# Performance work log

Measured on AMD Instinct MI355X. Metric: run time of the kernel, lower is better.

Reference implementation:

```python
import jax, jax.numpy as jnp
import numpy as np

V, D, H = 50000, 256, 4
HD = H * D            # concat head dim (TransformerConv concat=True)
HH, O = 256, 256      # invariant_hidden_dim, invariant_out_dim
B, N, E, L, A = 16, 1000, 4000, 64, 128
PAD = 0
SCALE = 1.0 / float(np.sqrt(D))


def emb_lookup(table, idx):
    # nn.Embedding with padding_idx: forward is a plain gather; grad at pad row is zeroed.
    rows = table[idx]
    return jnp.where((idx == PAD)[..., None], jax.lax.stop_gradient(rows), rows)


def transformer_conv(x, edge_index, ea, Wq, bq, Wk, bk, Wv, bv, We, Wskip, bskip):
    # PyG TransformerConv, heads=H, concat=True, root_weight=True, beta=False, dropout=0 (eval)
    n = x.shape[0]
    src, dst = edge_index[0], edge_index[1]
    q = (x @ Wq + bq).reshape(n, H, D)
    e = (ea @ We).reshape(-1, H, D)          # lin_edge (bias=False)
    k = (x @ Wk + bk).reshape(n, H, D)[src] + e
    v = (x @ Wv + bv).reshape(n, H, D)[src] + e
    alpha = (q[dst] * k).sum(-1) * SCALE      # [E,H]
    amax = jax.ops.segment_max(alpha, dst, num_segments=n)
    ex = jnp.exp(alpha - amax[dst])
    denom = jax.ops.segment_sum(ex, dst, num_segments=n)
    w = ex / denom[dst]                       # per-target-node softmax over incoming edges
    agg = jax.ops.segment_sum(v * w[..., None], dst, num_segments=n)
    return agg.reshape(n, HD) + x @ Wskip + bskip  # lin_skip on root


def mixed_embed(tok, node, graph_repr, emb):
    fixed = emb_lookup(emb, tok)
    flex = jnp.take_along_axis(graph_repr, node[..., None], axis=1)
    flex = jnp.where((node == PAD)[..., None], jax.lax.stop_gradient(flex), flex)
    return fixed + flex


def gru_last(xs, W_ih, W_hh, b_ih, b_hh):
    # torch nn.GRU, batch_first, 1 layer; only last hidden state is used
    gx = jnp.einsum('blh,gh->blg', xs, W_ih) + b_ih  # [B,L,3O]

    def step(h, g):
        gh = h @ W_hh.T + b_hh
        xr, xz, xn = jnp.split(g, 3, axis=-1)
        hr, hz, hn = jnp.split(gh, 3, axis=-1)
        r = jax.nn.sigmoid(xr + hr)
        z = jax.nn.sigmoid(xz + hz)
        c = jnp.tanh(xn + r * hn)
        return (1.0 - z) * c + z * h, None

    h0 = jnp.zeros((xs.shape[0], W_hh.shape[1]), xs.dtype)
    h_last, _ = jax.lax.scan(step, h0, jnp.swapaxes(gx, 0, 1))
    return h_last


def setup_inputs() -> dict:
    key = jax.random.key(0)
    ks = jax.random.split(key, 40)
    f = lambda i, shape, s=0.05: jax.random.normal(ks[i], shape, jnp.float32) * s
    ri = lambda i, shape, hi: jax.random.randint(ks[i], shape, 0, hi)
    return {
        'node_tokens': ri(0, (B, N), V),
        'edge_tokens': ri(1, (B, E), V),
        'edge_index': ri(2, (B, 2, E), N),
        'inv_token': ri(3, (B, L), V),
        'inv_node': ri(4, (B, L), N),
        'aa_token': ri(5, (B, A), V),
        'aa_node': ri(6, (B, A), N),
        'action_mask': jnp.ones((B, A), jnp.float32),
        'emb': f(7, (V, D), 0.02),
        'Wq': f(8, (D, HD)), 'bq': f(9, (HD,)),
        'Wk': f(10, (D, HD)), 'bk': f(11, (HD,)),
        'Wv': f(12, (D, HD)), 'bv': f(13, (HD,)),
        'We': f(14, (D, HD)),
        'Wskip': f(15, (D, HD)), 'bskip': f(16, (HD,)),
        'W1': f(17, (HD, D)), 'b1': f(18, (D,)),
        'Wp': f(19, (D, HH)), 'bp': f(20, (HH,)),
        'W_ih': f(21, (3 * O, HH)), 'W_hh': f(22, (3 * O, O)),
        'b_ih': f(23, (3 * O,)), 'b_hh': f(24, (3 * O,)),
        'Wab': f(25, (D, 1)), 'bab': f(26, (1,)),
        'Wap': f(27, (D, O)), 'bap': f(28, (O,)),
    }


def reference(node_tokens, edge_tokens, edge_index, inv_token, inv_node, aa_token, aa_node,
              action_mask, emb, Wq, bq, Wk, bk, Wv, bv, We, Wskip, bskip, W1, b1,
              Wp, bp, W_ih, W_hh, b_ih, b_hh, Wab, bab, Wap, bap):
    x = emb_lookup(emb, node_tokens)    # [B,N,D]
    ea = emb_lookup(emb, edge_tokens)   # [B,E,D]
    conv = jax.vmap(lambda xx, ei, ee: transformer_conv(
        xx, ei, ee, Wq, bq, Wk, bk, Wv, bv, We, Wskip, bskip))
    h = jax.nn.relu(conv(x, edge_index, ea))            # [B,N,HD]
    graph_repr = jax.nn.relu(h @ W1 + b1)               # [B,N,D]
    inv_h = jax.nn.relu(mixed_embed(inv_token, inv_node, graph_repr, emb) @ Wp + bp)
    inv = gru_last(inv_h, W_ih, W_hh, b_ih, b_hh)       # [B,O]
    aa_emb = mixed_embed(aa_token, aa_node, graph_repr, emb)  # [B,A,D]
    scores = jnp.einsum('bao,bo->ba', aa_emb @ Wap + bap, inv) + (aa_emb @ Wab + bab)[..., 0]
    inf_mask = jnp.maximum(jnp.log(action_mask), jnp.float32(np.finfo(np.float32).min))
    return scores + inf_mask
```

## Files before the change

kernel.cpp:

```cpp
#include <hip/hip_runtime.h>
#include <hip/hip_bf16.h>
#include <float.h>
#include <math.h>

typedef __hip_bfloat16 bf16;

#define B_ 16
#define N_ 1000
#define E_ 4000
#define L_ 64
#define A_ 128
#define D_ 256
#define H_ 4
#define HD_ 1024
#define SCALE_ 0.0625f

typedef __attribute__((ext_vector_type(8))) short short8;
typedef __attribute__((ext_vector_type(4))) float f32x4;

union U4S8 { uint4 u; short8 s; };

__device__ __forceinline__ unsigned short f2bf(float f) {
    bf16 h = __float2bfloat16(f);
    return *reinterpret_cast<unsigned short*>(&h);
}
__device__ __forceinline__ unsigned pack2(float a, float b) {
    return (unsigned)f2bf(a) | ((unsigned)f2bf(b) << 16);
}
__device__ __forceinline__ unsigned rne2(float a, float b) {
    unsigned ua = __float_as_uint(a), ub = __float_as_uint(b);
    ua += 0x7fff + ((ua >> 16) & 1);
    ub += 0x7fff + ((ub >> 16) & 1);
    return (ua >> 16) | (ub & 0xffff0000u);
}
__device__ __forceinline__ float bflo(unsigned u) { return __uint_as_float(u << 16); }
__device__ __forceinline__ float bfhi(unsigned u) { return __uint_as_float(u & 0xffff0000u); }

#define LOG2E 1.4426950408889634f
__device__ __forceinline__ float fsigm(float x) {
    return __builtin_amdgcn_rcpf(1.f + __builtin_amdgcn_exp2f(-LOG2E * x));
}
__device__ __forceinline__ float ftanh(float x) {
    return 1.f - 2.f * __builtin_amdgcn_rcpf(1.f + __builtin_amdgcn_exp2f(2.f * LOG2E * x));
}

__global__ void convemb_kernel(const float* __restrict__ src, bf16* __restrict__ dst, long n4)
{
    long i = (long)blockIdx.x * 256 + threadIdx.x;
    if (i >= n4) return;
    float4 v = *(const float4*)(src + i * 4);
    *(uint2*)(dst + i * 4) = make_uint2(pack2(v.x, v.y), pack2(v.z, v.w));
}

__global__ void pack_all_kernel(const float* __restrict__ Wq, const float* __restrict__ Wk,
                                const float* __restrict__ Wv, const float* __restrict__ Wskip,
                                const float* __restrict__ We, const float* __restrict__ W1,
                                const float* __restrict__ Wp, const float* __restrict__ W_ih,
                                const float* __restrict__ Wap, const float* __restrict__ W_hh,
                                const float* __restrict__ bq, const float* __restrict__ bk,
                                const float* __restrict__ bv, const float* __restrict__ bskip,
                                unsigned* __restrict__ qkvsP, unsigned* __restrict__ WeP,
                                unsigned* __restrict__ W1P, unsigned* __restrict__ WpP,
                                unsigned* __restrict__ WihP, unsigned* __restrict__ WapP,
                                short8* __restrict__ WhhP, float* __restrict__ bias4096)
{
    int i = blockIdx.x * 256 + threadIdx.x;
    if (i < 524288) {
        int k2 = i >> 12, n = i & 4095;
        const float* s = (n < 1024) ? Wq : (n < 2048) ? Wk : (n < 3072) ? Wv : Wskip;
        int col = n & 1023;
        qkvsP[i] = pack2(s[(long)(2 * k2) * 1024 + col], s[(long)(2 * k2 + 1) * 1024 + col]);
        return;
    }
    i -= 524288;
    if (i < 131072) {
        int k2 = i >> 10, n = i & 1023;
        WeP[i] = pack2(We[(long)(2 * k2) * 1024 + n], We[(long)(2 * k2 + 1) * 1024 + n]);
        return;
    }
    i -= 131072;
    if (i < 131072) {
        int k2 = i >> 8, n = i & 255;
        W1P[i] = pack2(W1[(long)(2 * k2) * 256 + n], W1[(long)(2 * k2 + 1) * 256 + n]);
        return;
    }
    i -= 131072;
    if (i < 32768) {
        int k2 = i >> 8, n = i & 255;
        WpP[i] = pack2(Wp[(long)(2 * k2) * 256 + n], Wp[(long)(2 * k2 + 1) * 256 + n]);
        return;
    }
    i -= 32768;
    if (i < 98304) {
        int k2 = i / 768, n = i % 768;
        WihP[i] = pack2(W_ih[(long)n * 256 + 2 * k2], W_ih[(long)n * 256 + 2 * k2 + 1]);
        return;
    }
    i -= 98304;
    if (i < 32768) {
        int k2 = i >> 8, n = i & 255;
        WapP[i] = pack2(Wap[(long)(2 * k2) * 256 + n], Wap[(long)(2 * k2 + 1) * 256 + n]);
        return;
    }
    i -= 32768;
    if (i < 24576) {
        int lane = i & 63, tk = (i >> 6) & 7, tile = i >> 9;
        int n = tile * 16 + (lane & 15);
        const float* wp = W_hh + (long)n * 256 + tk * 32 + (lane >> 4) * 8;
        float4 w0 = *(const float4*)wp;
        float4 w1 = *(const float4*)(wp + 4);
        U4S8 u;
        u.u = make_uint4(pack2(w0.x, w0.y), pack2(w0.z, w0.w),
                         pack2(w1.x, w1.y), pack2(w1.z, w1.w));
        WhhP[i] = u.s;
        return;
    }
    i -= 24576;
    if (i < 4096) {
        int q = i >> 10, c = i & 1023;
        bias4096[i] = ((q == 0) ? bq : (q == 1) ? bk : (q == 2) ? bv : bskip)[c];
    }
}
#define PACK_ALL_TOT (524288 + 131072 + 131072 + 32768 + 98304 + 32768 + 24576 + 4096)

#define TM 128
#define TN 128
#define TK 32
#define ASTR 40
#define BSTR 132

template <typename CT>
__global__ __launch_bounds__(256)
void pgemm_kernel(const bf16* __restrict__ A, const int* __restrict__ arows,
                  const unsigned* __restrict__ Bp, const float* __restrict__ bias,
                  CT* __restrict__ C, int M, int K, int Nc, int relu_out)
{
    __shared__ short    As[TM * ASTR];
    __shared__ unsigned Bs[(TK / 2) * BSTR];

    const int tid  = threadIdx.x;
    const int lane = tid & 63;
    const int wave = tid >> 6;
    const int wm = wave >> 1, wn = wave & 1;
    const int quad = lane >> 4, c16 = lane & 15;
    const long row0 = (long)blockIdx.y * TM;
    const int  col0 = blockIdx.x * TN;

    const int sm  = tid >> 1;
    const int sh  = (tid & 1) * 16;
    const int sn2 = tid & 63;
    const int skk = (tid >> 6) * 4;

    long gr_row = row0 + sm;
    if (gr_row > M - 1) gr_row = M - 1;
    long ar = arows ? (long)arows[gr_row] : gr_row;
    const short* Arow = (const short*)A + ar * K + sh;

    f32x4 acc[4][4];
    #pragma unroll
    for (int i = 0; i < 4; ++i)
        #pragma unroll
        for (int j = 0; j < 4; ++j)
            acc[i][j] = (f32x4){0.f, 0.f, 0.f, 0.f};

    for (int k0 = 0; k0 < K; k0 += TK) {
        {
            const short* p = Arow + k0;
            uint4 a = *(const uint4*)(p);
            uint4 b = *(const uint4*)(p + 8);
            *(uint4*)&As[sm * ASTR + sh]     = a;
            *(uint4*)&As[sm * ASTR + sh + 8] = b;
        }
        #pragma unroll
        for (int i = 0; i < 4; ++i) {
            int kk2 = skk + i;
            *(uint2*)&Bs[kk2 * BSTR + sn2 * 2] =
                *(const uint2*)&Bp[(long)(k0 / 2 + kk2) * Nc + col0 + sn2 * 2];
        }
        __syncthreads();

        short8 af[4];
        U4S8   bfr[4];
        #pragma unroll
        for (int mi = 0; mi < 4; ++mi) {
            int m = wm * 64 + mi * 16 + c16;
            af[mi] = *(const short8*)&As[m * ASTR + quad * 8];
        }
        #pragma unroll
        for (int ni = 0; ni < 4; ++ni) {
            int n = wn * 64 + ni * 16 + c16;
            uint4 u;
            u.x = Bs[(quad * 4 + 0) * BSTR + n];
            u.y = Bs[(quad * 4 + 1) * BSTR + n];
            u.z = Bs[(quad * 4 + 2) * BSTR + n];
            u.w = Bs[(quad * 4 + 3) * BSTR + n];
            bfr[ni].u = u;
        }
        #pragma unroll
        for (int mi = 0; mi < 4; ++mi)
            #pragma unroll
            for (int ni = 0; ni < 4; ++ni)
                acc[mi][ni] = __builtin_amdgcn_mfma_f32_16x16x32_bf16(
                    af[mi], bfr[ni].s, acc[mi][ni], 0, 0, 0);
        __syncthreads();
    }

    #pragma unroll
    for (int ni = 0; ni < 4; ++ni) {
        int col = col0 + wn * 64 + ni * 16 + c16;
        float bv = bias ? bias[col] : 0.f;
        #pragma unroll
        for (int mi = 0; mi < 4; ++mi) {
            long row = row0 + wm * 64 + mi * 16 + quad * 4;
            #pragma unroll
            for (int r = 0; r < 4; ++r) {
                if (row + r >= M) continue;
                float v = acc[mi][ni][r] + bv;
                if (relu_out) v = fmaxf(v, 0.f);
                C[(row + r) * Nc + col] = (CT)v;
            }
        }
    }
}

__global__ void zero_int_kernel(int* __restrict__ p, int n)
{
    int i = blockIdx.x * 256 + threadIdx.x;
    if (i < n) p[i] = 0;
}

__global__ void count_kernel(const int* __restrict__ edge_index, int b0,
                             int* __restrict__ cnt, int cE)
{
    int i = blockIdx.x * 256 + threadIdx.x;
    if (i >= cE) return;
    int bl = i / E_, ei = i % E_;
    int dst = edge_index[(long)(b0 + bl) * 2 * E_ + E_ + ei];
    atomicAdd(&cnt[bl * N_ + dst], 1);
}

__global__ __launch_bounds__(1024)
void scan_kernel(const int* __restrict__ cnt, int* __restrict__ row_start,
                 int* __restrict__ cursor)
{
    int bl = blockIdx.x;
    int tid = threadIdx.x;
    __shared__ int s[1024];
    int v = (tid < N_) ? cnt[bl * N_ + tid] : 0;
    s[tid] = v;
    __syncthreads();
    for (int off = 1; off < 1024; off <<= 1) {
        int t = (tid >= off) ? s[tid - off] : 0;
        __syncthreads();
        s[tid] += t;
        __syncthreads();
    }
    if (tid < N_) {
        int excl = s[tid] - v;
        row_start[bl * N_ + tid] = excl;
        cursor[bl * N_ + tid] = excl;
    }
}

__global__ void scatter_kernel(const int* __restrict__ edge_index, int b0,
                               int* __restrict__ cursor, int* __restrict__ elist, int cE)
{
    int i = blockIdx.x * 256 + threadIdx.x;
    if (i >= cE) return;
    int bl = i / E_, ei = i % E_;
    int dst = edge_index[(long)(b0 + bl) * 2 * E_ + E_ + ei];
    int pos = atomicAdd(&cursor[bl * N_ + dst], 1);
    elist[bl * E_ + pos] = ei;
}

__device__ __forceinline__ float qke2(unsigned q, unsigned k, unsigned e)
{
    return bflo(q) * (bflo(k) + bflo(e)) + bfhi(q) * (bfhi(k) + bfhi(e));
}

__global__ void alpha_ex_kernel(const bf16* __restrict__ qkvs, const bf16* __restrict__ e,
                                const int* __restrict__ edge_index,
                                int b0, float* __restrict__ ex, int cE)
{
    int eidx = blockIdx.x * 4 + (threadIdx.x >> 6);
    int l = threadIdx.x & 63;
    int bl = eidx / E_, ei = eidx % E_;
    const int* eb = edge_index + (long)(b0 + bl) * 2 * E_;
    int src = eb[ei], dst = eb[E_ + ei];
    int head = l >> 4;
    int j0 = head * 256 + (l & 15) * 16;

    const uint4* qp = (const uint4*)(qkvs + (long)(bl * N_ + dst) * 4096 + j0);
    const uint4* kp = (const uint4*)(qkvs + (long)(bl * N_ + src) * 4096 + 1024 + j0);
    const uint4* ep = (const uint4*)(e + (long)eidx * HD_ + j0);

    uint4 qa = qp[0], qb2 = qp[1];
    uint4 ka = kp[0], kb2 = kp[1];
    uint4 ea = ep[0], eb2 = ep[1];

    float s = qke2(qa.x, ka.x, ea.x) + qke2(qa.y, ka.y, ea.y)
            + qke2(qa.z, ka.z, ea.z) + qke2(qa.w, ka.w, ea.w)
            + qke2(qb2.x, kb2.x, eb2.x) + qke2(qb2.y, kb2.y, eb2.y)
            + qke2(qb2.z, kb2.z, eb2.z) + qke2(qb2.w, kb2.w, eb2.w);

    s += __shfl_down(s, 8);
    s += __shfl_down(s, 4);
    s += __shfl_down(s, 2);
    s += __shfl_down(s, 1);

    if ((l & 15) == 0)
        ex[(long)head * cE + eidx] = expf(s * SCALE_);
}

__global__ void agg_node_kernel(const bf16* __restrict__ qkvs, const bf16* __restrict__ e,
                                const float* __restrict__ ex, const int* __restrict__ edge_index,
                                const int* __restrict__ row_start, const int* __restrict__ cnt,
                                const int* __restrict__ elist,
                                int b0, int cE, bf16* __restrict__ aggb)
{
    int base = blockIdx.x;
    int bl = base / N_;
    int tid = threadIdx.x;
    int h = tid >> 6;
    int j0 = tid * 4;

    int start = row_start[base];
    int deg = cnt[base];
    const int* el = elist + (long)bl * E_;
    const float* exh = ex + (long)h * cE;
    const int* srcp = edge_index + (long)(b0 + bl) * 2 * E_;

    float d = 0.f;
    for (int t = 0; t < deg; ++t)
        d += exh[(long)bl * E_ + el[start + t]];
    float invd = (deg > 0) ? 1.f / d : 0.f;

    float a0 = 0.f, a1 = 0.f, a2 = 0.f, a3 = 0.f;
    for (int t = 0; t < deg; ++t) {
        int ei = el[start + t];
        long eidx = (long)bl * E_ + ei;
        float w = exh[eidx] * invd;
        int src = srcp[ei];
        uint2 vv = *(const uint2*)(qkvs + (long)(bl * N_ + src) * 4096 + 2048 + j0);
        uint2 ee = *(const uint2*)(e + eidx * HD_ + j0);
        a0 += w * (bflo(vv.x) + bflo(ee.x));
        a1 += w * (bfhi(vv.x) + bfhi(ee.x));
        a2 += w * (bflo(vv.y) + bflo(ee.y));
        a3 += w * (bfhi(vv.y) + bfhi(ee.y));
    }

    uint2 sk = *(const uint2*)(qkvs + (long)base * 4096 + 3072 + j0);
    unsigned o0 = pack2(fmaxf(bflo(sk.x) + a0, 0.f), fmaxf(bfhi(sk.x) + a1, 0.f));
    unsigned o1 = pack2(fmaxf(bflo(sk.y) + a2, 0.f), fmaxf(bfhi(sk.y) + a3, 0.f));
    *(uint2*)(aggb + (long)base * HD_ + j0) = make_uint2(o0, o1);
}

__global__ void mixed2_kernel(const bf16* __restrict__ embh,
                              const int* __restrict__ inv_token, const int* __restrict__ inv_node,
                              const int* __restrict__ aa_token, const int* __restrict__ aa_node,
                              const float* __restrict__ graph_repr,
                              bf16* __restrict__ mixed_inv, bf16* __restrict__ aa_emb)
{
    int r = blockIdx.x;
    int d = threadIdx.x;
    if (r < B_ * L_) {
        int b = r / L_;
        float v = (float)embh[(long)inv_token[r] * D_ + d] +
                  graph_repr[((long)b * N_ + inv_node[r]) * D_ + d];
        mixed_inv[(long)r * D_ + d] = __float2bfloat16(v);
    } else {
        int r2 = r - B_ * L_;
        int b = r2 / A_;
        float v = (float)embh[(long)aa_token[r2] * D_ + d] +
                  graph_repr[((long)b * N_ + aa_node[r2]) * D_ + d];
        aa_emb[(long)r2 * D_ + d] = __float2bfloat16(v);
    }
}

#define GSTR 780

__global__ __launch_bounds__(1024)
void gru_kernel(const bf16* __restrict__ gxh, const short8* __restrict__ WhhP,
                const float* __restrict__ b_hh, float* __restrict__ inv_out)
{
    __shared__ float gatesLDS[16 * GSTR];
    __shared__ short hB[16 * 264];

    const int tid = threadIdx.x;
    const int lane = tid & 63;
    const int wave = tid >> 6;
    const int quad = lane >> 4, col = lane & 15;

    for (int i = tid; i < 16 * 264; i += 1024) hB[i] = 0;

    short8 wfrag[3][8];
    float bhh[3];
    #pragma unroll
    for (int i = 0; i < 3; ++i) {
        int tile = wave * 3 + i;
        bhh[i] = b_hh[tile * 16 + col];
        #pragma unroll
        for (int tk = 0; tk < 8; ++tk)
            wfrag[i][tk] = WhhP[(tile * 8 + tk) * 64 + lane];
    }

    const int em = tid >> 6;
    const int c0 = (tid & 63) * 4;
    float myh0 = 0.f, myh1 = 0.f, myh2 = 0.f, myh3 = 0.f;

    const short* gbase = (const short*)gxh + (long)em * L_ * 768 + c0;

    uint2 pxr = *(const uint2*)(gbase);
    uint2 pxz = *(const uint2*)(gbase + 256);
    uint2 pxn = *(const uint2*)(gbase + 512);

    __syncthreads();

    for (int t = 0; t < L_; ++t) {
        uint2 xr2 = pxr, xz2 = pxz, xn2 = pxn;
        int nxt = (t + 1 < L_) ? t + 1 : t;
        const short* gp = gbase + (long)nxt * 768;
        pxr = *(const uint2*)(gp);
        pxz = *(const uint2*)(gp + 256);
        pxn = *(const uint2*)(gp + 512);

        f32x4 acc0 = (f32x4){bhh[0], bhh[0], bhh[0], bhh[0]};
        f32x4 acc1 = (f32x4){bhh[1], bhh[1], bhh[1], bhh[1]};
        f32x4 acc2 = (f32x4){bhh[2], bhh[2], bhh[2], bhh[2]};
        #pragma unroll
        for (int tk = 0; tk < 8; ++tk) {
            short8 a = *(const short8*)&hB[col * 264 + tk * 32 + quad * 8];
            acc0 = __builtin_amdgcn_mfma_f32_16x16x32_bf16(a, wfrag[0][tk], acc0, 0, 0, 0);
            acc1 = __builtin_amdgcn_mfma_f32_16x16x32_bf16(a, wfrag[1][tk], acc1, 0, 0, 0);
            acc2 = __builtin_amdgcn_mfma_f32_16x16x32_bf16(a, wfrag[2][tk], acc2, 0, 0, 0);
        }
        #pragma unroll
        for (int r = 0; r < 4; ++r) {
            int m = quad * 4 + r;
            gatesLDS[m * GSTR + (wave * 3 + 0) * 16 + col] = acc0[r];
            gatesLDS[m * GSTR + (wave * 3 + 1) * 16 + col] = acc1[r];
            gatesLDS[m * GSTR + (wave * 3 + 2) * 16 + col] = acc2[r];
        }
        __syncthreads();

        const float* g = &gatesLDS[em * GSTR + c0];
        float4 grv = *(const float4*)(g);
        float4 gzv = *(const float4*)(g + 256);
        float4 gnv = *(const float4*)(g + 512);
        float gr[4] = {grv.x, grv.y, grv.z, grv.w};
        float gz[4] = {gzv.x, gzv.y, gzv.z, gzv.w};
        float gn[4] = {gnv.x, gnv.y, gnv.z, gnv.w};
        float xr[4] = {bflo(xr2.x), bfhi(xr2.x), bflo(xr2.y), bfhi(xr2.y)};
        float xz[4] = {bflo(xz2.x), bfhi(xz2.x), bflo(xz2.y), bfhi(xz2.y)};
        float xn[4] = {bflo(xn2.x), bfhi(xn2.x), bflo(xn2.y), bfhi(xn2.y)};
        float hn[4];
        float hold[4] = {myh0, myh1, myh2, myh3};
        #pragma unroll
        for (int j = 0; j < 4; ++j) {
            float r = fsigm(xr[j] + gr[j]);
            float z = fsigm(xz[j] + gz[j]);
            float cc = ftanh(xn[j] + r * gn[j]);
            hn[j] = (1.f - z) * cc + z * hold[j];
        }
        myh0 = hn[0]; myh1 = hn[1]; myh2 = hn[2]; myh3 = hn[3];
        *(uint2*)&hB[em * 264 + c0] =
            make_uint2(rne2(hn[0], hn[1]), rne2(hn[2], hn[3]));
        __syncthreads();
    }

    float* op = inv_out + (long)em * 256 + c0;
    *(float4*)op = make_float4(myh0, myh1, myh2, myh3);
}

__global__ void score_kernel(const float* __restrict__ aa_p, const bf16* __restrict__ aa_emb,
                             const float* __restrict__ inv, const float* __restrict__ Wab,
                             const float* __restrict__ bab, const float* __restrict__ mask,
                             float* __restrict__ out)
{
    int r = blockIdx.x * 4 + (threadIdx.x >> 6);
    int l = threadIdx.x & 63;
    int b = r / A_;
    float s = 0.f;
    for (int d = l; d < D_; d += 64)
        s += aa_p[(long)r * D_ + d] * inv[(long)b * D_ + d] +
             (float)aa_emb[(long)r * D_ + d] * Wab[d];
    #pragma unroll
    for (int off = 32; off; off >>= 1) s += __shfl_down(s, off);
    if (l == 0) {
        float lm = logf(mask[r]);
        const float MN = -3.4028234663852886e38f;
        if (!(lm >= MN)) lm = MN;
        out[r] = s + bab[0] + lm;
    }
}

static inline size_t align256(size_t x) { return (x + 255) & ~(size_t)255; }

template <typename CT>
static void launch_pgemm(const bf16* A, const int* arows, const unsigned* Bp,
                         const float* bias, CT* C, int M, int K, int Nc, int relu,
                         hipStream_t s)
{
    dim3 grid(Nc / TN, (M + TM - 1) / TM);
    pgemm_kernel<CT><<<grid, 256, 0, s>>>(A, arows, Bp, bias, C, M, K, Nc, relu);
}

extern "C" void kernel_launch(void* const* d_in, const int* in_sizes, int n_in,
                              void* d_out, int out_size, void* d_ws, size_t ws_size,
                              hipStream_t stream)
{
    const int* node_tokens = (const int*)d_in[0];
    const int* edge_tokens = (const int*)d_in[1];
    const int* edge_index  = (const int*)d_in[2];
    const int* inv_token   = (const int*)d_in[3];
    const int* inv_node    = (const int*)d_in[4];
    const int* aa_token    = (const int*)d_in[5];
    const int* aa_node     = (const int*)d_in[6];
    const float* action_mask = (const float*)d_in[7];
    const float* emb   = (const float*)d_in[8];
    const float* Wq    = (const float*)d_in[9];
    const float* bq    = (const float*)d_in[10];
    const float* Wk    = (const float*)d_in[11];
    const float* bk    = (const float*)d_in[12];
    const float* Wv    = (const float*)d_in[13];
    const float* bv    = (const float*)d_in[14];
    const float* We    = (const float*)d_in[15];
    const float* Wskip = (const float*)d_in[16];
    const float* bskip = (const float*)d_in[17];
    const float* W1    = (const float*)d_in[18];
    const float* b1    = (const float*)d_in[19];
    const float* Wp    = (const float*)d_in[20];
    const float* bp    = (const float*)d_in[21];
    const float* W_ih  = (const float*)d_in[22];
    const float* W_hh  = (const float*)d_in[23];
    const float* b_ih  = (const float*)d_in[24];
    const float* b_hh  = (const float*)d_in[25];
    const float* Wab   = (const float*)d_in[26];
    const float* bab   = (const float*)d_in[27];
    const float* Wap   = (const float*)d_in[28];
    const float* bap   = (const float*)d_in[29];
    (void)in_sizes; (void)n_in; (void)out_size;

    char* base = (char*)d_ws;
    size_t off = 0;
    auto alloc = [&](size_t bytes) -> char* {
        char* p = base + off;
        off = align256(off + bytes);
        return p;
    };

    const long VD = 50000L * 256;
    bf16*  embh       = (bf16*)alloc(VD * 2);
    float* graph_repr = (float*)alloc((size_t)B_ * N_ * D_ * 4);
    bf16*  mixed_inv  = (bf16*)alloc((size_t)B_ * L_ * D_ * 2);
    bf16*  inv_h      = (bf16*)alloc((size_t)B_ * L_ * D_ * 2);
    bf16*  gxh        = (bf16*)alloc((size_t)B_ * L_ * 768 * 2);
    float* inv_out    = (float*)alloc((size_t)B_ * 256 * 4);
    bf16*  aa_emb     = (bf16*)alloc((size_t)B_ * A_ * D_ * 2);
    float* aa_p       = (float*)alloc((size_t)B_ * A_ * 256 * 4);
    unsigned* qkvsP   = (unsigned*)alloc((size_t)128 * 4096 * 4);
    unsigned* WeP     = (unsigned*)alloc((size_t)128 * 1024 * 4);
    unsigned* W1P     = (unsigned*)alloc((size_t)512 * 256 * 4);
    unsigned* WpP     = (unsigned*)alloc((size_t)128 * 256 * 4);
    unsigned* WihP    = (unsigned*)alloc((size_t)128 * 768 * 4);
    unsigned* WapP    = (unsigned*)alloc((size_t)128 * 256 * 4);
    short8* WhhP      = (short8*)alloc((size_t)24576 * 16);
    float* bias4096   = (float*)alloc(4096 * 4);
    size_t persist = off;

    int c = 16;
    while (c > 1) {
        size_t cN = (size_t)c * N_, cEs = (size_t)c * E_;
        size_t chunk = align256(cN * 4096 * 2)
                     + align256(cEs * HD_ * 2)
                     + align256(cN * HD_ * 2)
                     + align256(cEs * H_ * 4)
                     + 3 * align256(cN * 4)
                     + align256(cEs * 4);
        if (persist + chunk <= ws_size) break;
        c >>= 1;
    }
    int cN = c * N_, cE = c * E_;

    bf16*  qkvs  = (bf16*)alloc((size_t)cN * 4096 * 2);
    bf16*  ebuf  = (bf16*)alloc((size_t)cE * HD_ * 2);
    bf16*  aggb  = (bf16*)alloc((size_t)cN * HD_ * 2);
    float* ex    = (float*)alloc((size_t)cE * H_ * 4);
    int*   cnt   = (int*)alloc((size_t)cN * 4);
    int*   rstart= (int*)alloc((size_t)cN * 4);
    int*   cursor= (int*)alloc((size_t)cN * 4);
    int*   elist = (int*)alloc((size_t)cE * 4);

    convemb_kernel<<<(int)((VD / 4 + 255) / 256), 256, 0, stream>>>(emb, embh, VD / 4);
    pack_all_kernel<<<(PACK_ALL_TOT + 255) / 256, 256, 0, stream>>>(
        Wq, Wk, Wv, Wskip, We, W1, Wp, W_ih, Wap, W_hh, bq, bk, bv, bskip,
        qkvsP, WeP, W1P, WpP, WihP, WapP, WhhP, bias4096);

    for (int b0 = 0; b0 < B_; b0 += c) {
        zero_int_kernel<<<(cN + 255) / 256, 256, 0, stream>>>(cnt, cN);
        count_kernel<<<(cE + 255) / 256, 256, 0, stream>>>(edge_index, b0, cnt, cE);
        scan_kernel<<<c, 1024, 0, stream>>>(cnt, rstart, cursor);
        scatter_kernel<<<(cE + 255) / 256, 256, 0, stream>>>(edge_index, b0, cursor,
                                                             elist, cE);
        launch_pgemm<bf16>(embh, node_tokens + (long)b0 * N_, qkvsP, bias4096, qkvs,
                           cN, D_, 4096, 0, stream);
        launch_pgemm<bf16>(embh, edge_tokens + (long)b0 * E_, WeP, nullptr, ebuf,
                           cE, D_, HD_, 0, stream);
        alpha_ex_kernel<<<cE / 4, 256, 0, stream>>>(qkvs, ebuf, edge_index, b0, ex, cE);
        agg_node_kernel<<<cN, 256, 0, stream>>>(qkvs, ebuf, ex, edge_index, rstart, cnt,
                                                elist, b0, cE, aggb);
        launch_pgemm<float>(aggb, nullptr, W1P, b1,
                            graph_repr + (long)b0 * N_ * D_, cN, HD_, D_, 1, stream);
    }

    mixed2_kernel<<<B_ * L_ + B_ * A_, 256, 0, stream>>>(embh, inv_token, inv_node,
                                                         aa_token, aa_node, graph_repr,
                                                         mixed_inv, aa_emb);
    launch_pgemm<bf16>(mixed_inv, nullptr, WpP, bp, inv_h, B_ * L_, D_, 256, 1, stream);
    launch_pgemm<bf16>(inv_h, nullptr, WihP, b_ih, gxh, B_ * L_, 256, 768, 0, stream);
    gru_kernel<<<1, 1024, 0, stream>>>(gxh, WhhP, b_hh, inv_out);

    launch_pgemm<float>(aa_emb, nullptr, WapP, bap, aa_p, B_ * A_, D_, 256, 0, stream);
    score_kernel<<<(B_ * A_) / 4, 256, 0, stream>>>(aa_p, aa_emb, inv_out, Wab, bab,
                                                    action_mask, (float*)d_out);
}
```

Baseline: 906.9 us.

## Restructure GRU to compute gates in-register and double-buffer hidden state

The GRU kernel is reorganised so each wave owns matching r/z/n column tiles. Gate nonlinearities are then applied directly on the MFMA accumulators, which removes the gates LDS round trip and one of the two barriers per timestep. The hidden state is double-buffered in LDS, and a new transpose kernel lays out the input gates time-major with batch innermost to match the accumulator layout. The softmax exponential also switches from expf to the native exp2. This adds an extra launch and scattered 2-byte LDS writes.

```diff
diff --git a/kernel.cpp b/kernel.cpp
--- a/kernel.cpp
+++ b/kernel.cpp
@@ -27,11 +27,10 @@
 __device__ __forceinline__ unsigned pack2(float a, float b) {
     return (unsigned)f2bf(a) | ((unsigned)f2bf(b) << 16);
 }
-__device__ __forceinline__ unsigned rne2(float a, float b) {
-    unsigned ua = __float_as_uint(a), ub = __float_as_uint(b);
+__device__ __forceinline__ unsigned short rne1(float a) {
+    unsigned ua = __float_as_uint(a);
     ua += 0x7fff + ((ua >> 16) & 1);
-    ub += 0x7fff + ((ub >> 16) & 1);
-    return (ua >> 16) | (ub & 0xffff0000u);
+    return (unsigned short)(ua >> 16);
 }
 __device__ __forceinline__ float bflo(unsigned u) { return __uint_as_float(u << 16); }
 __device__ __forceinline__ float bfhi(unsigned u) { return __uint_as_float(u & 0xffff0000u); }
@@ -123,6 +122,16 @@
 }
 #define PACK_ALL_TOT (524288 + 131072 + 131072 + 32768 + 98304 + 32768 + 24576 + 4096)
 
+__global__ void gxt_kernel(const bf16* __restrict__ gxh, bf16* __restrict__ gxT)
+{
+    int i = blockIdx.x * 256 + threadIdx.x;
+    if (i >= B_ * L_ * 768) return;
+    int b = i / (L_ * 768);
+    int rem = i - b * (L_ * 768);
+    int t = rem / 768, n = rem - (rem / 768) * 768;
+    gxT[((long)t * 768 + n) * 16 + b] = gxh[i];
+}
+
 #define TM 128
 #define TN 128
 #define TK 32
@@ -309,7 +318,7 @@
     s += __shfl_down(s, 1);
 
     if ((l & 15) == 0)
-        ex[(long)head * cE + eidx] = expf(s * SCALE_);
+        ex[(long)head * cE + eidx] = __builtin_amdgcn_exp2f(s * (SCALE_ * LOG2E));
 }
 
 __global__ void agg_node_kernel(const bf16* __restrict__ qkvs, const bf16* __restrict__ e,
@@ -377,99 +386,86 @@
     }
 }
 
-#define GSTR 780
-
 __global__ __launch_bounds__(1024)
-void gru_kernel(const bf16* __restrict__ gxh, const short8* __restrict__ WhhP,
+void gru_kernel(const bf16* __restrict__ gxT, const short8* __restrict__ WhhP,
                 const float* __restrict__ b_hh, float* __restrict__ inv_out)
 {
-    __shared__ float gatesLDS[16 * GSTR];
-    __shared__ short hB[16 * 264];
+    __shared__ short hB[2][16 * 264];
 
     const int tid = threadIdx.x;
     const int lane = tid & 63;
     const int wave = tid >> 6;
-    const int quad = lane >> 4, col = lane & 15;
-
-    for (int i = tid; i < 16 * 264; i += 1024) hB[i] = 0;
-
-    short8 wfrag[3][8];
-    float bhh[3];
+    const int quad = lane >> 4, c16 = lane & 15;
+    const int n0 = wave * 16 + c16;
+
+    for (int i = tid; i < 2 * 16 * 264; i += 1024) ((short*)hB)[i] = 0;
+
+    short8 wfr[8], wfz[8], wfn[8];
     #pragma unroll
-    for (int i = 0; i < 3; ++i) {
-        int tile = wave * 3 + i;
-        bhh[i] = b_hh[tile * 16 + col];
-        #pragma unroll
-        for (int tk = 0; tk < 8; ++tk)
-            wfrag[i][tk] = WhhP[(tile * 8 + tk) * 64 + lane];
-    }
-
-    const int em = tid >> 6;
-    const int c0 = (tid & 63) * 4;
+    for (int tk = 0; tk < 8; ++tk) {
+        wfr[tk] = WhhP[((0 * 16 + wave) * 8 + tk) * 64 + lane];
+        wfz[tk] = WhhP[((1 * 16 + wave) * 8 + tk) * 64 + lane];
+        wfn[tk] = WhhP[((2 * 16 + wave) * 8 + tk) * 64 + lane];
+    }
+    float bhr = b_hh[0 * 256 + n0];
+    float bhz = b_hh[1 * 256 + n0];
+    float bhn = b_hh[2 * 256 + n0];
+
     float myh0 = 0.f, myh1 = 0.f, myh2 = 0.f, myh3 = 0.f;
 
-    const short* gbase = (const short*)gxh + (long)em * L_ * 768 + c0;
-
-    uint2 pxr = *(const uint2*)(gbase);
-    uint2 pxz = *(const uint2*)(gbase + 256);
-    uint2 pxn = *(const uint2*)(gbase + 512);
+    const short* gbr = (const short*)gxT + (long)(0 * 256 + n0) * 16 + quad * 4;
+    const short* gbz = gbr + 256 * 16;
+    const short* gbn = gbr + 512 * 16;
+
+    uint2 pxr = *(const uint2*)gbr;
+    uint2 pxz = *(const uint2*)gbz;
+    uint2 pxn = *(const uint2*)gbn;
 
     __syncthreads();
 
+    int p = 0;
     for (int t = 0; t < L_; ++t) {
         uint2 xr2 = pxr, xz2 = pxz, xn2 = pxn;
-        int nxt = (t + 1 < L_) ? t + 1 : t;
-        const short* gp = gbase + (long)nxt * 768;
-        pxr = *(const uint2*)(gp);
-        pxz = *(const uint2*)(gp + 256);
-        pxn = *(const uint2*)(gp + 512);
-
-        f32x4 acc0 = (f32x4){bhh[0], bhh[0], bhh[0], bhh[0]};
-        f32x4 acc1 = (f32x4){bhh[1], bhh[1], bhh[1], bhh[1]};
-        f32x4 acc2 = (f32x4){bhh[2], bhh[2], bhh[2], bhh[2]};
+        long noff = (long)((t + 1 < L_) ? t + 1 : t) * 12288;
+        pxr = *(const uint2*)(gbr + noff);
+        pxz = *(const uint2*)(gbz + noff);
+        pxn = *(const uint2*)(gbn + noff);
+
+        f32x4 ar = (f32x4){bhr, bhr, bhr, bhr};
+        f32x4 az = (f32x4){bhz, bhz, bhz, bhz};
+        f32x4 an = (f32x4){bhn, bhn, bhn, bhn};
+        const short* hp = &hB[p][0];
         #pragma unroll
         for (int tk = 0; tk < 8; ++tk) {
-            short8 a = *(const short8*)&hB[col * 264 + tk * 32 + quad * 8];
-            acc0 = __builtin_amdgcn_mfma_f32_16x16x32_bf16(a, wfrag[0][tk], acc0, 0, 0, 0);
-            acc1 = __builtin_amdgcn_mfma_f32_16x16x32_bf16(a, wfrag[1][tk], acc1, 0, 0, 0);
-            acc2 = __builtin_amdgcn_mfma_f32_16x16x32_bf16(a, wfrag[2][tk], acc2, 0, 0, 0);
+            short8 a = *(const short8*)&hp[c16 * 264 + tk * 32 + quad * 8];
+            ar = __builtin_amdgcn_mfma_f32_16x16x32_bf16(a, wfr[tk], ar, 0, 0, 0);
+            az = __builtin_amdgcn_mfma_f32_16x16x32_bf16(a, wfz[tk], az, 0, 0, 0);
+            an = __builtin_amdgcn_mfma_f32_16x16x32_bf16(a, wfn[tk], an, 0, 0, 0);
         }
-        #pragma unroll
-        for (int r = 0; r < 4; ++r) {
-            int m = quad * 4 + r;
-            gatesLDS[m * GSTR + (wave * 3 + 0) * 16 + col] = acc0[r];
-            gatesLDS[m * GSTR + (wave * 3 + 1) * 16 + col] = acc1[r];
-            gatesLDS[m * GSTR + (wave * 3 + 2) * 16 + col] = acc2[r];
-        }
-        __syncthreads();
-
-        const float* g = &gatesLDS[em * GSTR + c0];
-        float4 grv = *(const float4*)(g);
-        float4 gzv = *(const float4*)(g + 256);
-        float4 gnv = *(const float4*)(g + 512);
-        float gr[4] = {grv.x, grv.y, grv.z, grv.w};
-        float gz[4] = {gzv.x, gzv.y, gzv.z, gzv.w};
-        float gn[4] = {gnv.x, gnv.y, gnv.z, gnv.w};
+
         float xr[4] = {bflo(xr2.x), bfhi(xr2.x), bflo(xr2.y), bfhi(xr2.y)};
         float xz[4] = {bflo(xz2.x), bfhi(xz2.x), bflo(xz2.y), bfhi(xz2.y)};
         float xn[4] = {bflo(xn2.x), bfhi(xn2.x), bflo(xn2.y), bfhi(xn2.y)};
+        float hold[4] = {myh0, myh1, myh2, myh3};
         float hn[4];
-        float hold[4] = {myh0, myh1, myh2, myh3};
-        #pragma unroll
-        for (int j = 0; j < 4; ++j) {
-            float r = fsigm(xr[j] + gr[j]);
-            float z = fsigm(xz[j] + gz[j]);
-            float cc = ftanh(xn[j] + r * gn[j]);
-            hn[j] = (1.f - z) * cc + z * hold[j];
+        short* hw = &hB[p ^ 1][0];
+        #pragma unroll
+        for (int r = 0; r < 4; ++r) {
+            float rr = fsigm(xr[r] + ar[r]);
+            float zz = fsigm(xz[r] + az[r]);
+            float cc = ftanh(xn[r] + rr * an[r]);
+            hn[r] = (1.f - zz) * cc + zz * hold[r];
+            hw[(quad * 4 + r) * 264 + n0] = (short)rne1(hn[r]);
         }
         myh0 = hn[0]; myh1 = hn[1]; myh2 = hn[2]; myh3 = hn[3];
-        *(uint2*)&hB[em * 264 + c0] =
-            make_uint2(rne2(hn[0], hn[1]), rne2(hn[2], hn[3]));
+        p ^= 1;
         __syncthreads();
     }
 
-    float* op = inv_out + (long)em * 256 + c0;
-    *(float4*)op = make_float4(myh0, myh1, myh2, myh3);
+    inv_out[(long)(quad * 4 + 0) * 256 + n0] = myh0;
+    inv_out[(long)(quad * 4 + 1) * 256 + n0] = myh1;
+    inv_out[(long)(quad * 4 + 2) * 256 + n0] = myh2;
+    inv_out[(long)(quad * 4 + 3) * 256 + n0] = myh3;
 }
 
 __global__ void score_kernel(const float* __restrict__ aa_p, const bf16* __restrict__ aa_emb,
@@ -555,6 +551,7 @@
     bf16*  mixed_inv  = (bf16*)alloc((size_t)B_ * L_ * D_ * 2);
     bf16*  inv_h      = (bf16*)alloc((size_t)B_ * L_ * D_ * 2);
     bf16*  gxh        = (bf16*)alloc((size_t)B_ * L_ * 768 * 2);
+    bf16*  gxT        = (bf16*)alloc((size_t)B_ * L_ * 768 * 2);
     float* inv_out    = (float*)alloc((size_t)B_ * 256 * 4);
     bf16*  aa_emb     = (bf16*)alloc((size_t)B_ * A_ * D_ * 2);
     float* aa_p       = (float*)alloc((size_t)B_ * A_ * 256 * 4);
@@ -618,7 +615,8 @@
                                                          mixed_inv, aa_emb);
     launch_pgemm<bf16>(mixed_inv, nullptr, WpP, bp, inv_h, B_ * L_, D_, 256, 1, stream);
     launch_pgemm<bf16>(inv_h, nullptr, WihP, b_ih, gxh, B_ * L_, 256, 768, 0, stream);
-    gru_kernel<<<1, 1024, 0, stream>>>(gxh, WhhP, b_hh, inv_out);
+    gxt_kernel<<<(B_ * L_ * 768 + 255) / 256, 256, 0, stream>>>(gxh, gxT);
+    gru_kernel<<<1, 1024, 0, stream>>>(gxT, WhhP, b_hh, inv_out);
 
     launch_pgemm<float>(aa_emb, nullptr, WapP, bap, aa_p, B_ * A_, D_, 256, 0, stream);
     score_kernel<<<(B_ * A_) / 4, 256, 0, stream>>>(aa_p, aa_emb, inv_out, Wab, bab,
```

Measured after the change: 888.4 us. 2.0% less time.
